# Performance work log

Measured on AMD Instinct MI355X. Metric: run time of the kernel, lower is better.

Reference implementation:

```python
import jax, jax.numpy as jnp
import numpy as np

EPS = 1e-5
B, CIN, COUT, H, W = 32, 512, 512, 56, 56
K = 4            # kernel_num
A = 32           # attention_channel = max(int(512*0.0625), 16)


def setup_inputs() -> dict:
    key = jax.random.key(0)
    ks = jax.random.split(key, 16)
    s = lambda fan: 1.0 / np.sqrt(fan)
    return {
        "x": jax.random.normal(ks[0], (B, CIN, H, W), jnp.float32),
        # attention trunk: global-avgpool -> fc -> bn -> relu
        "fc_w": jax.random.normal(ks[1], (A, CIN), jnp.float32) * s(CIN),
        "abn_g": jnp.ones((A,), jnp.float32),
        "abn_b": jnp.zeros((A,), jnp.float32),
        "abn_m": jax.random.normal(ks[2], (A,), jnp.float32) * 0.1,
        "abn_v": jax.random.uniform(ks[3], (A,), jnp.float32, 0.5, 1.5),
        # channel / filter / kernel attention heads
        "ch_w": jax.random.normal(ks[4], (CIN, A), jnp.float32) * s(A),
        "ch_b": jnp.zeros((CIN,), jnp.float32),
        "fl_w": jax.random.normal(ks[5], (COUT, A), jnp.float32) * s(A),
        "fl_b": jnp.zeros((COUT,), jnp.float32),
        "kn_w": jax.random.normal(ks[6], (K, A), jnp.float32) * s(A),
        "kn_b": jnp.zeros((K,), jnp.float32),
        # base 1x1 conv weight bank [kernel_num, out, in] (1x1 spatial squeezed)
        "weight": jax.random.normal(ks[7], (K, COUT, CIN), jnp.float32) * s(CIN),
        # output BatchNorm2d (eval mode: running stats)
        "bn_g": jnp.ones((COUT,), jnp.float32),
        "bn_b": jnp.zeros((COUT,), jnp.float32),
        "bn_m": jax.random.normal(ks[8], (COUT,), jnp.float32) * 0.1,
        "bn_v": jax.random.uniform(ks[9], (COUT,), jnp.float32, 0.5, 1.5),
    }


def reference(x, fc_w, abn_g, abn_b, abn_m, abn_v,
              ch_w, ch_b, fl_w, fl_b, kn_w, kn_b,
              weight, bn_g, bn_b, bn_m, bn_v):
    # ---- omni-dimensional attention (kernel_size=1 => spatial attn skipped) ----
    pooled = jnp.mean(x, axis=(2, 3))                       # [B, Cin]
    h = pooled @ fc_w.T                                     # [B, A]
    h = (h - abn_m) * (abn_g / jnp.sqrt(abn_v + EPS)) + abn_b
    h = jax.nn.relu(h)
    ch_att = jax.nn.sigmoid(h @ ch_w.T + ch_b)              # [B, Cin]
    fl_att = jax.nn.sigmoid(h @ fl_w.T + fl_b)              # [B, Cout]
    kn_att = jax.nn.softmax(h @ kn_w.T + kn_b, axis=1)      # [B, K] (temperature=1)
    # ---- per-sample aggregated 1x1 kernel + grouped(batch) pointwise conv ----
    agg_w = jnp.einsum('bk,koc->boc', kn_att, weight)       # [B, Cout, Cin]
    xm = x * ch_att[:, :, None, None]                       # channel attention
    y = jnp.einsum('bchw,boc->bohw', xm, agg_w)             # batched 1x1 conv
    y = y * fl_att[:, :, None, None]                        # filter attention
    # ---- BatchNorm2d (inference) ----
    inv = bn_g / jnp.sqrt(bn_v + EPS)
    y = (y - bn_m[None, :, None, None]) * inv[None, :, None, None] + bn_b[None, :, None, None]
    return y
```

## Files before the change

kernel.cpp:

```cpp
#include <hip/hip_runtime.h>
#include <math.h>

#define BATCH 32
#define CIN   512
#define COUT  512
#define HW    3136
#define KNUM  4
#define ADIM  32
#define EPS   1e-5f

static constexpr size_t XT_OFF    = 0;
static constexpr size_t WF_OFF    = 102760448;
static constexpr size_t PART_OFF  = 119537664;
static constexpr size_t CH_OFF    = 122748928;
static constexpr size_t FLINV_OFF = 122814464;
static constexpr size_t KN_OFF    = 122880000;

typedef __attribute__((ext_vector_type(8))) short short8;
typedef __attribute__((ext_vector_type(4))) float float4v;

typedef const unsigned int __attribute__((address_space(1)))* gas_ptr;
typedef unsigned int __attribute__((address_space(3)))* lds_ptr;

__device__ __forceinline__ unsigned short f2bf(float f) {
  unsigned int u = __float_as_uint(f);
  u += 0x7FFFu + ((u >> 16) & 1u);
  return (unsigned short)(u >> 16);
}

__global__ __launch_bounds__(256) void transpose_pool(
    const float* __restrict__ x, unsigned short* __restrict__ xT,
    float* __restrict__ part) {
  __shared__ unsigned short T[64 * 128];
  const int pb = blockIdx.x * 64;
  const int cb = blockIdx.y * 128;
  const int b  = blockIdx.z;
  const int t  = threadIdx.x;
  const int pq = t & 15;
  const int ch = t >> 4;

  float s[4][2];
  #pragma unroll
  for (int it = 0; it < 4; ++it) {
    const int cp = it * 16 + ch;
    const int c  = cb + cp * 2;
    const float* xp = x + (size_t)(b * CIN + c) * HW + pb + pq * 4;
    float4 v0 = *(const float4*)(xp);
    float4 v1 = *(const float4*)(xp + HW);
    s[it][0] = v0.x + v0.y + v0.z + v0.w;
    s[it][1] = v1.x + v1.y + v1.z + v1.w;
    const int dbase = (((cp >> 2) ^ pq) & 15) * 4 + (cp & 3);
    const float* f0 = (const float*)&v0;
    const float* f1 = (const float*)&v1;
    #pragma unroll
    for (int j = 0; j < 4; ++j) {
      const int p = pq * 4 + j;
      unsigned int w = (unsigned int)f2bf(f0[j]) |
                       ((unsigned int)f2bf(f1[j]) << 16);
      *(unsigned int*)&T[p * 128 + dbase * 2] = w;
    }
  }
  #pragma unroll
  for (int it = 0; it < 4; ++it) {
    #pragma unroll
    for (int e = 0; e < 2; ++e) {
      float v = s[it][e];
      #pragma unroll
      for (int off = 8; off > 0; off >>= 1) v += __shfl_down(v, off, 16);
      if (pq == 0)
        part[((size_t)b * 49 + blockIdx.x) * 512 + cb + (it * 16 + ch) * 2 + e] = v;
    }
  }
  __syncthreads();
  const int cg = t & 15;
  const int rb = t >> 4;
  #pragma unroll
  for (int itr = 0; itr < 4; ++itr) {
    const int p = rb + itr * 16;
    const int key = (p >> 2) & 15;
    uint4 r = *(const uint4*)&T[p * 128 + ((cg ^ key) & 15) * 8];
    *(uint4*)(xT + (size_t)(b * HW + pb + p) * CIN + cb + cg * 8) = r;
  }
}

__global__ __launch_bounds__(256) void attn_all(
    const float* __restrict__ part, const float* __restrict__ fc_w,
    const float* __restrict__ abn_g, const float* __restrict__ abn_b,
    const float* __restrict__ abn_m, const float* __restrict__ abn_v,
    const float* __restrict__ kn_w, const float* __restrict__ kn_b,
    const float* __restrict__ ch_w, const float* __restrict__ ch_b,
    const float* __restrict__ fl_w, const float* __restrict__ fl_b,
    const float* __restrict__ bn_g, const float* __restrict__ bn_v,
    float* __restrict__ ch_out, float* __restrict__ flinv_out,
    float* __restrict__ kn_out) {
  __shared__ float pooledS[CIN];
  __shared__ float hs[ADIM];
  const int b = blockIdx.x, t = threadIdx.x;
  #pragma unroll
  for (int idx = t; idx < CIN; idx += 256) {
    float s = 0.f;
    for (int j = 0; j < 49; ++j) s += part[((size_t)b * 49 + j) * 512 + idx];
    pooledS[idx] = s;
  }
  __syncthreads();
  {
    const int a = t >> 3, pz = t & 7;
    const float* fr = fc_w + a * CIN + pz * 64;
    const float* pp = pooledS + pz * 64;
    float s = 0.f;
    #pragma unroll 8
    for (int c = 0; c < 64; ++c) s += pp[c] * fr[c];
    #pragma unroll
    for (int off = 4; off > 0; off >>= 1) s += __shfl_down(s, off, 8);
    if (pz == 0) {
      s *= (1.0f / (float)HW);
      float vv = (s - abn_m[a]) * (abn_g[a] * rsqrtf(abn_v[a] + EPS)) + abn_b[a];
      hs[a] = fmaxf(vv, 0.f);
    }
  }
  __syncthreads();
  if (t == 0) {
    float lg[KNUM]; float mx = -1e30f;
    for (int k = 0; k < KNUM; ++k) {
      float acc = kn_b[k];
      for (int aa = 0; aa < ADIM; ++aa) acc += hs[aa] * kn_w[k * ADIM + aa];
      lg[k] = acc; mx = fmaxf(mx, acc);
    }
    float ssum = 0.f;
    for (int k = 0; k < KNUM; ++k) { lg[k] = expf(lg[k] - mx); ssum += lg[k]; }
    for (int k = 0; k < KNUM; ++k) kn_out[b * KNUM + k] = lg[k] / ssum;
  }
  #pragma unroll
  for (int c = t; c < CIN; c += 256) {
    const float* wr = ch_w + c * ADIM;
    float acc = ch_b[c];
    #pragma unroll
    for (int aa = 0; aa < ADIM; ++aa) acc += hs[aa] * wr[aa];
    ch_out[b * CIN + c] = 1.f / (1.f + expf(-acc));
  }
  #pragma unroll
  for (int o = t; o < COUT; o += 256) {
    const float* wr = fl_w + o * ADIM;
    float acc = fl_b[o];
    #pragma unroll
    for (int aa = 0; aa < ADIM; ++aa) acc += hs[aa] * wr[aa];
    float sig = 1.f / (1.f + expf(-acc));
    flinv_out[b * COUT + o] = sig * (bn_g[o] * rsqrtf(bn_v[o] + EPS));
  }
}

__global__ __launch_bounds__(256) void build_wf(
    const float* __restrict__ weight, const float* __restrict__ kn,
    const float* __restrict__ ch, const float* __restrict__ flinv,
    unsigned short* __restrict__ Wf) {
  const int och = blockIdx.x, b = blockIdx.y, t = threadIdx.x;
  const int o0 = och * 16;
  const float k0 = kn[b * KNUM + 0], k1 = kn[b * KNUM + 1];
  const float k2 = kn[b * KNUM + 2], k3 = kn[b * KNUM + 3];
  #pragma unroll
  for (int i = 0; i < 8; ++i) {
    int cell = i * 1024 + t * 4;
    int ol = cell >> 9, c = cell & 511;
    int o = o0 + ol;
    float fi = flinv[b * COUT + o];
    const float* wp = weight + (size_t)o * CIN + c;
    float4 w0 = *(const float4*)(wp);
    float4 w1 = *(const float4*)(wp + 1 * CIN * COUT);
    float4 w2 = *(const float4*)(wp + 2 * CIN * COUT);
    float4 w3 = *(const float4*)(wp + 3 * CIN * COUT);
    float4 cv = *(const float4*)(ch + b * CIN + c);
    ushort4 r;
    r.x = f2bf((k0 * w0.x + k1 * w1.x + k2 * w2.x + k3 * w3.x) * cv.x * fi);
    r.y = f2bf((k0 * w0.y + k1 * w1.y + k2 * w2.y + k3 * w3.y) * cv.y * fi);
    r.z = f2bf((k0 * w0.z + k1 * w1.z + k2 * w2.z + k3 * w3.z) * cv.z * fi);
    r.w = f2bf((k0 * w0.w + k1 * w1.w + k2 * w2.w + k3 * w3.w) * cv.w * fi);
    *(ushort4*)(Wf + (size_t)(b * COUT + o) * CIN + c) = r;
  }
}

__global__ __launch_bounds__(256, 4) void gemm_kernel(
    const unsigned short* __restrict__ xT, const unsigned short* __restrict__ Wf,
    const float* __restrict__ bn_g, const float* __restrict__ bn_b,
    const float* __restrict__ bn_m, const float* __restrict__ bn_v,
    float* __restrict__ y) {
  __shared__ unsigned short lA[128 * 64];
  __shared__ unsigned short lB[128 * 64];
  const int ot = blockIdx.x, pt = blockIdx.y, b = blockIdx.z;
  const int o0 = ot * 128, p0 = pt * 128;
  const int t = threadIdx.x;
  const int wave = t >> 6, lane = t & 63;
  const int wm = wave & 1, wn = wave >> 1;

  const int srow = lane >> 3;
  const int sgrp = lane & 7;
  const int scol = ((sgrp ^ srow) * 8);

  const unsigned short* Ab = Wf + (size_t)b * COUT * CIN;
  const unsigned short* Bb = xT + (size_t)b * HW * CIN;
  const unsigned short* aSrc[4];
  const unsigned short* bSrc[4];
  #pragma unroll
  for (int q = 0; q < 4; ++q) {
    const int ar = o0 + wave * 32 + q * 8 + srow;
    aSrc[q] = Ab + (size_t)ar * CIN + scol;
    int br = p0 + wave * 32 + q * 8 + srow;
    if (br > HW - 1) br = HW - 1;
    bSrc[q] = Bb + (size_t)br * CIN + scol;
  }

  float4v acc[4][4];
  #pragma unroll
  for (int i = 0; i < 4; ++i)
    #pragma unroll
    for (int j = 0; j < 4; ++j)
      #pragma unroll
      for (int r = 0; r < 4; ++r) acc[i][j][r] = 0.f;

  const int arow = lane & 15;
  const int kgrp = lane >> 4;
  const int slot0 = ((0 + kgrp) ^ (arow & 7)) * 8;
  const int slot1 = ((4 + kgrp) ^ (arow & 7)) * 8;

  for (int kt = 0; kt < CIN / 64; ++kt) {
    const int c0 = kt * 64;
    __syncthreads();
    #pragma unroll
    for (int q = 0; q < 4; ++q) {
      __builtin_amdgcn_global_load_lds((gas_ptr)(const void*)(aSrc[q] + c0),
          (lds_ptr)(void*)&lA[(wave * 32 + q * 8) * 64], 16, 0, 0);
      __builtin_amdgcn_global_load_lds((gas_ptr)(const void*)(bSrc[q] + c0),
          (lds_ptr)(void*)&lB[(wave * 32 + q * 8) * 64], 16, 0, 0);
    }
    __syncthreads();

    #pragma unroll
    for (int ks = 0; ks < 2; ++ks) {
      const int sl = ks ? slot1 : slot0;
      short8 af[4], bfr[4];
      #pragma unroll
      for (int i = 0; i < 4; ++i)
        af[i] = *(const short8*)&lA[(wm * 64 + i * 16 + arow) * 64 + sl];
      #pragma unroll
      for (int j = 0; j < 4; ++j)
        bfr[j] = *(const short8*)&lB[(wn * 64 + j * 16 + arow) * 64 + sl];
      #pragma unroll
      for (int i = 0; i < 4; ++i)
        #pragma unroll
        for (int j = 0; j < 4; ++j)
          acc[i][j] = __builtin_amdgcn_mfma_f32_16x16x32_bf16(af[i], bfr[j], acc[i][j], 0, 0, 0);
    }
  }

  const int rowq = (lane >> 4) * 4;
  const int coln = lane & 15;
  #pragma unroll
  for (int i = 0; i < 4; ++i) {
    const int obase = o0 + wm * 64 + i * 16 + rowq;
    float bet[4];
    #pragma unroll
    for (int r = 0; r < 4; ++r) {
      const int o = obase + r;
      const float inv = bn_g[o] * rsqrtf(bn_v[o] + EPS);
      bet[r] = bn_b[o] - bn_m[o] * inv;
    }
    #pragma unroll
    for (int j = 0; j < 4; ++j) {
      const int p = p0 + wn * 64 + j * 16 + coln;
      if (p < HW) {
        #pragma unroll
        for (int r = 0; r < 4; ++r)
          y[(size_t)(b * COUT + obase + r) * HW + p] = acc[i][j][r] + bet[r];
      }
    }
  }
}

extern "C" void kernel_launch(void* const* d_in, const int* in_sizes, int n_in,
                              void* d_out, int out_size, void* d_ws, size_t ws_size,
                              hipStream_t stream) {
  (void)in_sizes; (void)n_in; (void)out_size; (void)ws_size;
  const float* x     = (const float*)d_in[0];
  const float* fc_w  = (const float*)d_in[1];
  const float* abn_g = (const float*)d_in[2];
  const float* abn_b = (const float*)d_in[3];
  const float* abn_m = (const float*)d_in[4];
  const float* abn_v = (const float*)d_in[5];
  const float* ch_w  = (const float*)d_in[6];
  const float* ch_b  = (const float*)d_in[7];
  const float* fl_w  = (const float*)d_in[8];
  const float* fl_b  = (const float*)d_in[9];
  const float* kn_w  = (const float*)d_in[10];
  const float* kn_b  = (const float*)d_in[11];
  const float* weight= (const float*)d_in[12];
  const float* bn_g  = (const float*)d_in[13];
  const float* bn_b  = (const float*)d_in[14];
  const float* bn_m  = (const float*)d_in[15];
  const float* bn_v  = (const float*)d_in[16];
  float* out = (float*)d_out;

  char* ws = (char*)d_ws;
  unsigned short* xT = (unsigned short*)(ws + XT_OFF);
  unsigned short* Wf = (unsigned short*)(ws + WF_OFF);
  float* part  = (float*)(ws + PART_OFF);
  float* ch    = (float*)(ws + CH_OFF);
  float* flinv = (float*)(ws + FLINV_OFF);
  float* kn    = (float*)(ws + KN_OFF);

  transpose_pool<<<dim3(49, 4, BATCH), 256, 0, stream>>>(x, xT, part);
  attn_all<<<BATCH, 256, 0, stream>>>(part, fc_w, abn_g, abn_b, abn_m, abn_v,
                                      kn_w, kn_b, ch_w, ch_b, fl_w, fl_b,
                                      bn_g, bn_v, ch, flinv, kn);
  build_wf<<<dim3(32, BATCH), 256, 0, stream>>>(weight, kn, ch, flinv, Wf);
  gemm_kernel<<<dim3(4, 25, BATCH), 256, 0, stream>>>(xT, Wf, bn_g, bn_b, bn_m, bn_v, out);
}
```

Baseline: 491.4 us.

## Restructure GEMM into 256x256 tiles with 4-stage LDS pipeline and XCD-aware block remap

The batched GEMM now uses 512-thread blocks computing 256x256 output tiles with K-steps of 32. A four-buffer ring in 128KB of dynamic LDS keeps three stages of global_load_lds in flight, synchronised by explicit vmcnt waits, in place of the old single-buffer load/sync/compute loop. The change also adds a 1D grid remapped across the 8 XCDs, s_setprio around the MFMA burst, and a new swizzle for the 32-wide K tiles. The aim is to hide global-load latency and raise data reuse per block. The cost is higher register pressure from 128 accumulators per thread and fewer resident blocks because of the large LDS footprint.

```diff
diff --git a/kernel.cpp b/kernel.cpp
--- a/kernel.cpp
+++ b/kernel.cpp
@@ -21,6 +21,9 @@
 
 typedef const unsigned int __attribute__((address_space(1)))* gas_ptr;
 typedef unsigned int __attribute__((address_space(3)))* lds_ptr;
+
+#define WAITVM(N) asm volatile("s_waitcnt vmcnt(" #N ")" ::: "memory")
+#define BARRIER() do { __builtin_amdgcn_s_barrier(); asm volatile("" ::: "memory"); } while (0)
 
 __device__ __forceinline__ unsigned short f2bf(float f) {
   unsigned int u = __float_as_uint(f);
@@ -178,39 +181,44 @@
   }
 }
 
-__global__ __launch_bounds__(256, 4) void gemm_kernel(
+__global__ __launch_bounds__(512, 2) void gemm_kernel(
     const unsigned short* __restrict__ xT, const unsigned short* __restrict__ Wf,
     const float* __restrict__ bn_g, const float* __restrict__ bn_b,
     const float* __restrict__ bn_m, const float* __restrict__ bn_v,
     float* __restrict__ y) {
-  __shared__ unsigned short lA[128 * 64];
-  __shared__ unsigned short lB[128 * 64];
-  const int ot = blockIdx.x, pt = blockIdx.y, b = blockIdx.z;
-  const int o0 = ot * 128, p0 = pt * 128;
+  extern __shared__ unsigned short L[];
+  const int id = blockIdx.x;
+  const int wg = (id & 7) * 104 + (id >> 3);
+  const int ot = wg & 1;
+  const int rem = wg >> 1;
+  const int pt = rem % 13;
+  const int b  = rem / 13;
+  const int o0 = ot * 256, p0 = pt * 256;
   const int t = threadIdx.x;
   const int wave = t >> 6, lane = t & 63;
-  const int wm = wave & 1, wn = wave >> 1;
-
-  const int srow = lane >> 3;
-  const int sgrp = lane & 7;
-  const int scol = ((sgrp ^ srow) * 8);
+  const int wm = wave >> 2, wn = wave & 3;
 
   const unsigned short* Ab = Wf + (size_t)b * COUT * CIN;
   const unsigned short* Bb = xT + (size_t)b * HW * CIN;
-  const unsigned short* aSrc[4];
-  const unsigned short* bSrc[4];
-  #pragma unroll
-  for (int q = 0; q < 4; ++q) {
-    const int ar = o0 + wave * 32 + q * 8 + srow;
-    aSrc[q] = Ab + (size_t)ar * CIN + scol;
-    int br = p0 + wave * 32 + q * 8 + srow;
-    if (br > HW - 1) br = HW - 1;
-    bSrc[q] = Bb + (size_t)br * CIN + scol;
-  }
-
-  float4v acc[4][4];
-  #pragma unroll
-  for (int i = 0; i < 4; ++i)
+
+  const int rr = lane >> 2;
+  const int gp = (lane & 3) ^ ((lane >> 3) & 3);
+  const unsigned short* aS[2];
+  const unsigned short* bS[2];
+  int dOff[2];
+  #pragma unroll
+  for (int q = 0; q < 2; ++q) {
+    const int m = q * 8 + wave;
+    dOff[q] = m * 512;
+    aS[q] = Ab + (size_t)(o0 + m * 16 + rr) * CIN + gp * 8;
+    int brow = p0 + m * 16 + rr;
+    if (brow > HW - 1) brow = HW - 1;
+    bS[q] = Bb + (size_t)brow * CIN + gp * 8;
+  }
+
+  float4v acc[8][4];
+  #pragma unroll
+  for (int i = 0; i < 8; ++i)
     #pragma unroll
     for (int j = 0; j < 4; ++j)
       #pragma unroll
@@ -218,44 +226,58 @@
 
   const int arow = lane & 15;
   const int kgrp = lane >> 4;
-  const int slot0 = ((0 + kgrp) ^ (arow & 7)) * 8;
-  const int slot1 = ((4 + kgrp) ^ (arow & 7)) * 8;
-
-  for (int kt = 0; kt < CIN / 64; ++kt) {
-    const int c0 = kt * 64;
-    __syncthreads();
-    #pragma unroll
-    for (int q = 0; q < 4; ++q) {
-      __builtin_amdgcn_global_load_lds((gas_ptr)(const void*)(aSrc[q] + c0),
-          (lds_ptr)(void*)&lA[(wave * 32 + q * 8) * 64], 16, 0, 0);
-      __builtin_amdgcn_global_load_lds((gas_ptr)(const void*)(bSrc[q] + c0),
-          (lds_ptr)(void*)&lB[(wave * 32 + q * 8) * 64], 16, 0, 0);
-    }
-    __syncthreads();
-
-    #pragma unroll
-    for (int ks = 0; ks < 2; ++ks) {
-      const int sl = ks ? slot1 : slot0;
-      short8 af[4], bfr[4];
-      #pragma unroll
-      for (int i = 0; i < 4; ++i)
-        af[i] = *(const short8*)&lA[(wm * 64 + i * 16 + arow) * 64 + sl];
+  const int sl = (kgrp ^ ((arow >> 1) & 3)) * 8;
+
+  auto stage = [&](int tt) {
+    const int bufb = (tt & 3) * 16384;
+    const int co = tt * 32;
+    #pragma unroll
+    for (int q = 0; q < 2; ++q)
+      __builtin_amdgcn_global_load_lds((gas_ptr)(const void*)(aS[q] + co),
+          (lds_ptr)(void*)&L[bufb + dOff[q]], 16, 0, 0);
+    #pragma unroll
+    for (int q = 0; q < 2; ++q)
+      __builtin_amdgcn_global_load_lds((gas_ptr)(const void*)(bS[q] + co),
+          (lds_ptr)(void*)&L[bufb + 8192 + dOff[q]], 16, 0, 0);
+  };
+
+  auto compute = [&](int tt) {
+    const int bufb = (tt & 3) * 16384;
+    short8 af[8], bv[4];
+    #pragma unroll
+    for (int i = 0; i < 8; ++i)
+      af[i] = *(const short8*)&L[bufb + (wm * 128 + i * 16 + arow) * 32 + sl];
+    #pragma unroll
+    for (int j = 0; j < 4; ++j)
+      bv[j] = *(const short8*)&L[bufb + 8192 + (wn * 64 + j * 16 + arow) * 32 + sl];
+    __builtin_amdgcn_s_setprio(1);
+    #pragma unroll
+    for (int i = 0; i < 8; ++i)
       #pragma unroll
       for (int j = 0; j < 4; ++j)
-        bfr[j] = *(const short8*)&lB[(wn * 64 + j * 16 + arow) * 64 + sl];
-      #pragma unroll
-      for (int i = 0; i < 4; ++i)
-        #pragma unroll
-        for (int j = 0; j < 4; ++j)
-          acc[i][j] = __builtin_amdgcn_mfma_f32_16x16x32_bf16(af[i], bfr[j], acc[i][j], 0, 0, 0);
-    }
-  }
+        acc[i][j] = __builtin_amdgcn_mfma_f32_16x16x32_bf16(af[i], bv[j], acc[i][j], 0, 0, 0);
+    __builtin_amdgcn_s_setprio(0);
+  };
+
+  stage(0); stage(1); stage(2);
+  WAITVM(8);
+  BARRIER();
+  #pragma unroll 1
+  for (int tt = 0; tt < 13; ++tt) {
+    stage(tt + 3);
+    compute(tt);
+    WAITVM(8);
+    BARRIER();
+  }
+  compute(13); WAITVM(4); BARRIER();
+  compute(14); WAITVM(0); BARRIER();
+  compute(15);
 
   const int rowq = (lane >> 4) * 4;
   const int coln = lane & 15;
   #pragma unroll
-  for (int i = 0; i < 4; ++i) {
-    const int obase = o0 + wm * 64 + i * 16 + rowq;
+  for (int i = 0; i < 8; ++i) {
+    const int obase = o0 + wm * 128 + i * 16 + rowq;
     float bet[4];
     #pragma unroll
     for (int r = 0; r < 4; ++r) {
@@ -306,10 +328,17 @@
   float* flinv = (float*)(ws + FLINV_OFF);
   float* kn    = (float*)(ws + KN_OFF);
 
+  static bool attr_done = false;
+  if (!attr_done) {
+    hipFuncSetAttribute((const void*)gemm_kernel,
+                        hipFuncAttributeMaxDynamicSharedMemorySize, 131072);
+    attr_done = true;
+  }
+
   transpose_pool<<<dim3(49, 4, BATCH), 256, 0, stream>>>(x, xT, part);
   attn_all<<<BATCH, 256, 0, stream>>>(part, fc_w, abn_g, abn_b, abn_m, abn_v,
                                       kn_w, kn_b, ch_w, ch_b, fl_w, fl_b,
                                       bn_g, bn_v, ch, flinv, kn);
   build_wf<<<dim3(32, BATCH), 256, 0, stream>>>(weight, kn, ch, flinv, Wf);
-  gemm_kernel<<<dim3(4, 25, BATCH), 256, 0, stream>>>(xT, Wf, bn_g, bn_b, bn_m, bn_v, out);
-}
+  gemm_kernel<<<dim3(832), dim3(512), 131072, stream>>>(xT, Wf, bn_g, bn_b, bn_m, bn_v, out);
+}
```

Result: no change. 485.4 us (-1.2%).
